# Optimization experiments

Measured on AMD Instinct MI355X. Metric: run time of the kernel, lower is better.

## Reference

```python
import jax, jax.numpy as jnp
import numpy as np

D = 128; T = 128; E = 100; H = 2
B = 2048; N0 = 3 * B; K0 = 5; N1 = N0 * K0; K1 = 10
NN = 200000; M = 4096; MSG = 2 * D + E + T  # 484


def t2v(t, w, b):
    # Time2Vec: cos(t * w + b), output [..., T]
    return jnp.cos(t[..., None] * w + b)


def gru_cell(x, h, Wih, bih, Whh, bhh):
    gi = x @ Wih.T + bih
    gh = h @ Whh.T + bhh
    ir, iz, inn = jnp.split(gi, 3, axis=-1)
    hr, hz, hn = jnp.split(gh, 3, axis=-1)
    r = jax.nn.sigmoid(ir + hr)
    u = jax.nn.sigmoid(iz + hz)
    n = jnp.tanh(inn + r * hn)
    return (1.0 - u) * n + u * h


def temporal_attn(node_feat, time_feat, edge_feat, nbr_feat, nbr_time_feat, mask,
                  Wq, bq, Wk, bk, Wv, bv, Wo, bo):
    N = node_feat.shape[0]
    q = (jnp.concatenate([node_feat, time_feat], -1) @ Wq + bq).reshape(N, H, D // H)
    kin = jnp.concatenate([nbr_feat, edge_feat, nbr_time_feat], -1)  # [N, K, D+E+T]
    k = (kin @ Wk + bk).reshape(N, -1, H, D // H)
    v = (kin @ Wv + bv).reshape(N, -1, H, D // H)
    s = jnp.einsum('nhd,nkhd->nhk', q, k) / jnp.sqrt(jnp.asarray(D // H, q.dtype))
    s = jnp.where(mask[:, None, :] > 0, s, jnp.asarray(-1e9, s.dtype))
    a = jax.nn.softmax(s, axis=-1)
    hout = jnp.einsum('nhk,nkhd->nhd', a, v).reshape(N, D)
    return jax.nn.relu(jnp.concatenate([hout, node_feat], -1) @ Wo + bo)


def setup_inputs() -> dict:
    key = jax.random.key(0)
    ks = jax.random.split(key, 60)
    it = iter(range(60))
    nx = lambda: ks[next(it)]
    p = lambda shape: jax.random.normal(nx(), shape, jnp.float32) * 0.05
    inp = dict(memory=p((NN, D)), time_w=p((T,)), time_b=p((T,)),
               gru_Wih=p((3 * D, MSG)), gru_bih=p((3 * D,)),
               gru_Whh=p((3 * D, D)), gru_bhh=p((3 * D,)))
    for l in (0, 1):
        inp['Wq%d' % l] = p((D + T, D)); inp['bq%d' % l] = p((D,))
        inp['Wk%d' % l] = p((D + E + T, D)); inp['bk%d' % l] = p((D,))
        inp['Wv%d' % l] = p((D + E + T, D)); inp['bv%d' % l] = p((D,))
        inp['Wo%d' % l] = p((2 * D, D)); inp['bo%d' % l] = p((D,))
    inp.update(lp_Ws=p((D, D)), lp_bs=p((D,)), lp_Wd=p((D, D)), lp_bd=p((D,)),
               lp_Wo=p((D, 1)), lp_bo=p((1,)))
    inp['msgs'] = jax.random.normal(nx(), (M, MSG), jnp.float32)
    inp['times0'] = jax.random.uniform(nx(), (N0,), jnp.float32) * 100.0 + 100.0
    inp['nbr_times0'] = inp['times0'][:, None] - jax.random.uniform(nx(), (N0, K0), jnp.float32) * 100.0
    inp['nbr_feats0'] = jax.random.normal(nx(), (N0, K0, E), jnp.float32)
    inp['times1'] = jax.random.uniform(nx(), (N1,), jnp.float32) * 100.0 + 100.0
    inp['nbr_times1'] = inp['times1'][:, None] - jax.random.uniform(nx(), (N1, K1), jnp.float32) * 100.0
    inp['nbr_feats1'] = jax.random.normal(nx(), (N1, K1, E), jnp.float32)
    inp['msg_nids'] = jax.random.permutation(nx(), NN)[:M].astype(jnp.int32)
    inp['seed0'] = jax.random.randint(nx(), (N0,), 0, NN, jnp.int32)
    inp['seed1'] = jax.random.randint(nx(), (N1,), 0, NN, jnp.int32)
    inp['nbr_local0'] = (N0 + jax.random.randint(nx(), (N0, K0), 0, N1)).astype(jnp.int32)
    inp['nbr_mask0'] = jax.random.randint(nx(), (N0, K0), 0, 2, jnp.int32).at[:, 0].set(1)
    inp['nbr_mask1'] = jax.random.randint(nx(), (N1, K1), 0, 2, jnp.int32).at[:, 0].set(1)
    inp['src_local'] = jax.random.randint(nx(), (B,), 0, N0, jnp.int32)
    inp['dst_local'] = jax.random.randint(nx(), (B,), 0, N0, jnp.int32)
    inp['neg_local'] = jax.random.randint(nx(), (B,), 0, N0, jnp.int32)
    return inp


def reference(memory, time_w, time_b, gru_Wih, gru_bih, gru_Whh, gru_bhh,
              Wq0, bq0, Wk0, bk0, Wv0, bv0, Wo0, bo0,
              Wq1, bq1, Wk1, bk1, Wv1, bv1, Wo1, bo1,
              lp_Ws, lp_bs, lp_Wd, lp_bd, lp_Wo, lp_bo,
              msgs, times0, nbr_times0, nbr_feats0, times1, nbr_times1, nbr_feats1,
              msg_nids, seed0, seed1, nbr_local0, nbr_mask0, nbr_mask1,
              src_local, dst_local, neg_local):
    # GRU memory update on aggregated messages (get_updated_memory)
    mem = memory.at[msg_nids].set(
        gru_cell(msgs, memory[msg_nids], gru_Wih, gru_bih, gru_Whh, gru_bhh))
    z = jnp.zeros((N0 + N1, D), jnp.float32)
    # hop 1 (outermost): neighbor node features are zeros
    tf1 = t2v(jnp.zeros((N1,), jnp.float32), time_w, time_b)
    ntf1 = t2v(times1[:, None] - nbr_times1, time_w, time_b)
    out1 = temporal_attn(mem[seed1], tf1, nbr_feats1,
                         jnp.zeros((N1, K1, D), jnp.float32), ntf1, nbr_mask1,
                         Wq1, bq1, Wk1, bk1, Wv1, bv1, Wo1, bo1)
    z = z.at[N0 + jnp.arange(N1)].set(out1)
    # hop 0: gather neighbor embeddings from hop-1 results
    tf0 = t2v(jnp.zeros((N0,), jnp.float32), time_w, time_b)
    ntf0 = t2v(times0[:, None] - nbr_times0, time_w, time_b)
    out0 = temporal_attn(mem[seed0], tf0, nbr_feats0, z[nbr_local0], ntf0, nbr_mask0,
                         Wq0, bq0, Wk0, bk0, Wv0, bv0, Wo0, bo0)
    z = z.at[jnp.arange(N0)].set(out0)
    z_src, z_dst, z_neg = z[src_local], z[dst_local], z[neg_local]

    def link_pred(a, c):
        hh = jax.nn.relu(a @ lp_Ws + lp_bs + c @ lp_Wd + lp_bd)
        return jax.nn.sigmoid(hh @ lp_Wo + lp_bo).ravel()

    return link_pred(z_src, z_dst), link_pred(z_src, z_neg)
```

## Files before the change

### kernel.cpp

```cpp
#include <hip/hip_runtime.h>
#include <math.h>

#define D    128
#define TT   128
#define E    100
#define NHD  2
#define BSZ  2048
#define N0C  6144
#define K0C  5
#define N1C  30720
#define K1C  10
#define NNC  200000
#define MC   4096
#define MSG  484
#define KIN  356
#define GK   612
#define GKP  616
#define GN   512

typedef __attribute__((ext_vector_type(8))) short short8v;
typedef __attribute__((ext_vector_type(4))) float f32x4;

__device__ __forceinline__ float sigmoidf_(float x){ return 1.f/(1.f+__expf(-x)); }
__device__ __forceinline__ unsigned short f2b(float f){
    unsigned int x = __float_as_uint(f);
    unsigned int r = (x + 0x7fffu + ((x>>16)&1u)) >> 16;
    return (unsigned short)r;
}
__device__ __forceinline__ float b2f(unsigned short u){
    return __uint_as_float(((unsigned int)u)<<16);
}

__global__ void k_pre_small(const float* time_b,
                            const float* Wq0,const float* bq0,const float* Wq1,const float* bq1,
                            const float* bv0,const float* Wo0,const float* bo0,
                            const float* bv1,const float* Wo1,const float* bo1,
                            float* qc0, float* qc1, float* cb0, float* cb1){
    __shared__ float cosb[TT];
    int j = threadIdx.x;
    cosb[j] = cosf(time_b[j]);
    __syncthreads();
    float a0=bq0[j], a1=bq1[j];
    for(int t=0;t<TT;++t){ a0 += cosb[t]*Wq0[(D+t)*D + j]; a1 += cosb[t]*Wq1[(D+t)*D + j]; }
    qc0[j]=a0; qc1[j]=a1;
    float c0=bo0[j], c1=bo1[j];
    for(int jp=0;jp<D;++jp){ c0 += bv0[jp]*Wo0[jp*D + j]; c1 += bv1[jp]*Wo1[jp*D + j]; }
    cb0[j]=c0; cb1[j]=c1;
}

__global__ void k_wf(const float* Wq,const float* Wk,const float* bk,const float* qc,
                     unsigned short* WF, float* cF, int cmin){
    int span = 356 - cmin;
    int hstr = span + 4;
    int width = 2*hstr;
    int idx = blockIdx.x;
    int h = idx / hstr; int cl = idx % hstr;
    int k = threadIdx.x;
    if(cl > span){
        WF[(size_t)k*width + idx] = (unsigned short)0;
        if(k==0) cF[idx] = 0.f;
        return;
    }
    int c = cmin + cl;
    float a = 0.f;
    for(int d=0; d<64; ++d){
        float wkv = (c < KIN) ? Wk[c*D + h*64+d] : bk[h*64+d];
        a += Wq[k*D + h*64+d] * wkv;
    }
    WF[(size_t)k*width + idx] = f2b(a);
    if(k==0){
        float s=0.f;
        for(int d=0; d<64; ++d){
            float wkv = (c < KIN) ? Wk[c*D + h*64+d] : bk[h*64+d];
            s += qc[h*64+d]*wkv;
        }
        cF[idx] = s;
    }
}

__global__ void k_bcat(const float* Wv, const float* Wo, unsigned short* Bcat, int cmin){
    int span = KIN - cmin; int rows = 2*span;
    int r = blockIdx.x; int j = threadIdx.x;
    float a;
    if(r < rows){
        int h = r/span; int c = cmin + (r - h*span);
        a = 0.f;
        for(int d=0; d<64; ++d) a += Wv[c*D + h*64+d] * Wo[(h*64+d)*D + j];
    } else {
        a = Wo[(size_t)(D + (r - rows))*D + j];
    }
    Bcat[(size_t)r*D + j] = f2b(a);
}

__global__ __launch_bounds__(256) void k_gruB(const float* Wih, const float* Whh, unsigned short* B){
    __shared__ float tile[64][65];
    int rb = blockIdx.x*64;
    int jb = blockIdx.y*64;
    int t = threadIdx.x;
    int rr = t&63, jj0 = t>>6;
    #pragma unroll
    for(int i=0;i<16;++i){
        int jj = jj0 + i*4;
        int j = jb + jj; int r = rb + rr;
        float v = 0.f;
        if(r < GK){
            if(j < 256)      v = (r<MSG)? Wih[(size_t)j*MSG+r] : Whh[(size_t)j*D + (r-MSG)];
            else if(j < 384) v = (r<MSG)? Wih[(size_t)j*MSG+r] : 0.f;
            else             v = (r<MSG)? 0.f : Whh[(size_t)(j-128)*D + (r-MSG)];
        }
        tile[jj][rr] = v;
    }
    __syncthreads();
    int jw = t&63, rr0 = t>>6;
    #pragma unroll
    for(int i=0;i<16;++i){
        int rr2 = rr0 + i*4;
        int r = rb + rr2;
        if(r < GK) B[(size_t)r*GN + jb + jw] = f2b(tile[jw][rr2]);
    }
}
__global__ void k_gruBias(const float* bih, const float* bhh, float* bias){
    int j = threadIdx.x + blockIdx.x*256;
    if(j >= GN) return;
    float v;
    if(j < 256)      v = bih[j] + bhh[j];
    else if(j < 384) v = bih[j];
    else             v = bhh[j-128];
    bias[j] = v;
}
__global__ void k_acvt(const float* msgs, const float* memory, const int* msg_nids,
                       unsigned short* ab, float* hprevf){
    int i = blockIdx.x*256 + threadIdx.x;
    if(i >= MC*GKP) return;
    int row = i / GKP; int c = i - row*GKP;
    float v;
    if(c < MSG) v = msgs[(size_t)row*MSG + c];
    else if(c < GK){ int d = c-MSG; v = memory[(size_t)msg_nids[row]*D + d]; hprevf[row*D+d] = v; }
    else v = 0.f;
    ab[i] = f2b(v);
}
__global__ void k_gates3(const float* part, const float* bias, const float* hprevf, float* upd){
    int i = blockIdx.x*256 + threadIdx.x;
    if(i >= MC*D) return;
    int row = i>>7, d = i&127;
    const float* p = part + (size_t)row*GN;
    const size_t S = (size_t)MC*GN;
    float gr = p[d]     + p[S+d]     + p[2*S+d]     + bias[d];
    float gu = p[128+d] + p[S+128+d] + p[2*S+128+d] + bias[128+d];
    float gi = p[256+d] + p[S+256+d] + p[2*S+256+d] + bias[256+d];
    float gh = p[384+d] + p[S+384+d] + p[2*S+384+d] + bias[384+d];
    float r = sigmoidf_(gr);
    float u = sigmoidf_(gu);
    float n = tanhf(gi + r*gh);
    upd[i] = (1.f-u)*n + u*hprevf[i];
}

__global__ void k_map_init(int* map){ int i = blockIdx.x*256+threadIdx.x; if(i<NNC) map[i] = -1; }
__global__ void k_map_scatter(const int* msg_nids, int* map){
    int i = blockIdx.x*256+threadIdx.x; if(i<MC) map[msg_nids[i]] = i;
}

__global__ void k_gatherf(const int* seed1,const int* seed0,const int* map,
                          const float* memory,const float* upd,
                          unsigned short* hb1, unsigned short* acat1,
                          unsigned short* hb0, unsigned short* acat0){
    int i = blockIdx.x*256 + threadIdx.x;
    const int total1 = N1C*D;
    int li; const int* seed; unsigned short* hb; unsigned short* acat; int ldav, hoff;
    if(i < total1){ li=i; seed=seed1; hb=hb1; acat=acat1; ldav=584; hoff=456; }
    else { li = i - total1; if(li >= N0C*D) return; seed=seed0; hb=hb0; acat=acat0; ldav=840; hoff=712; }
    int row = li>>7, c = li&127;
    int sid = seed[row];
    int mi = map[sid];
    float v = (mi>=0) ? upd[(size_t)mi*D + c] : memory[(size_t)sid*D + c];
    unsigned short u = f2b(v);
    hb[li] = u;
    acat[(size_t)row*ldav + hoff + c] = u;
}

template<int BM, int SPLITK, bool RELU, bool OUTF32>
__global__ __launch_bounds__(256) void k_gmm(const unsigned short* A, int lda,
                                             const unsigned short* B, int ldb,
                                             const float* bias, void* Cp, int ldc,
                                             int K, int N, int M){
    constexpr int ASTR = 72;
    constexpr int BSTR = 72;
    constexpr int RPW = BM/4;
    constexpr int RT  = RPW/16;
    constexpr int AIT = BM/32;
    __shared__ unsigned short As[BM*ASTR];
    __shared__ unsigned short Bs[64*BSTR];
    int t = threadIdx.x;
    int wave = t>>6, lane = t&63;
    int l15 = lane&15, l4 = lane>>4;
    int m0 = blockIdx.y*BM, n0 = blockIdx.x*64;
    int ntiles = (K+63)>>6;
    int tbeg, tend;
    if(SPLITK==1){ tbeg=0; tend=ntiles; }
    else {
        int tper = (ntiles + SPLITK-1)/SPLITK;
        tbeg = blockIdx.z*tper;
        tend = min(ntiles, tbeg+tper);
    }
    f32x4 acc[RT][4];
    #pragma unroll
    for(int rt=0;rt<RT;++rt)
        #pragma unroll
        for(int ct=0;ct<4;++ct) acc[rt][ct] = (f32x4){0.f,0.f,0.f,0.f};

    uint4 apre[AIT]; unsigned short bpre[16];
    auto loadA = [&](int kt){
        int k0 = kt<<6;
        #pragma unroll
        for(int i=0;i<AIT;++i){
            int idx = t + i*256;
            int row = idx>>3; int kc = (idx&7)*8;
            uint4 v = {0u,0u,0u,0u};
            if(k0+kc < K) v = *(const uint4*)(A + (size_t)(m0+row)*lda + k0 + kc);
            apre[i] = v;
        }
    };
    auto loadB = [&](int kt){
        int k0 = kt<<6;
        int n = t&63; int kb = (t>>6)*16;
        int ng = n0+n;
        #pragma unroll
        for(int j=0;j<16;++j){
            int kg = k0 + kb + j;
            bpre[j] = (kg<K && ng<N) ? B[(size_t)kg*ldb + ng] : (unsigned short)0;
        }
    };
    auto stash = [&](){
        #pragma unroll
        for(int i=0;i<AIT;++i){
            int idx = t + i*256;
            int row = idx>>3; int kc = (idx&7)*8;
            *(uint4*)&As[row*ASTR + kc] = apre[i];
        }
        int n = t&63; int kb = (t>>6)*16;
        #pragma unroll
        for(int j=0;j<16;++j) Bs[n*BSTR + kb + j] = bpre[j];
    };

    loadA(tbeg); loadB(tbeg);
    for(int kt=tbeg; kt<tend; ++kt){
        stash();
        __syncthreads();
        if(kt+1 < tend){ loadA(kt+1); loadB(kt+1); }
        #pragma unroll
        for(int kk=0; kk<64; kk+=32){
            short8v bfr[4];
            #pragma unroll
            for(int ct=0;ct<4;++ct)
                bfr[ct] = *(const short8v*)&Bs[(ct*16+l15)*BSTR + kk + l4*8];
            #pragma unroll
            for(int rt=0;rt<RT;++rt){
                short8v afr = *(const short8v*)&As[(wave*RPW + rt*16 + l15)*ASTR + kk + l4*8];
                #pragma unroll
                for(int ct=0;ct<4;++ct)
                    acc[rt][ct] = __builtin_amdgcn_mfma_f32_16x16x32_bf16(afr, bfr[ct], acc[rt][ct], 0,0,0);
            }
        }
        __syncthreads();
    }
    #pragma unroll
    for(int rt=0;rt<RT;++rt){
        #pragma unroll
        for(int ct=0;ct<4;++ct){
            int col = n0 + ct*16 + l15;
            if(col < N){
                #pragma unroll
                for(int r=0;r<4;++r){
                    int row = m0 + wave*RPW + rt*16 + l4*4 + r;
                    if(SPLITK==1){
                        float v = acc[rt][ct][r] + bias[col];
                        if(RELU) v = fmaxf(v, 0.f);
                        if(OUTF32) ((float*)Cp)[(size_t)row*ldc + col] = v;
                        else ((unsigned short*)Cp)[(size_t)row*ldc + col] = f2b(v);
                    } else {
                        ((float*)Cp)[((size_t)blockIdx.z*M + row)*ldc + col] = acc[rt][ct][r];
                    }
                }
            }
        }
    }
}

template<int SPL, bool RELU, bool OUTF32>
__global__ void k_kred(const float* part, int M, int N, const float* bias, void* out){
    int i = blockIdx.x*256 + threadIdx.x;
    if(i >= M*N) return;
    int col = i & (N-1);
    float v = bias[col];
    #pragma unroll
    for(int z=0;z<SPL;++z) v += part[(size_t)z*M*N + i];
    if(RELU) v = fmaxf(v, 0.f);
    if(OUTF32) ((float*)out)[i] = v;
    else ((unsigned short*)out)[i] = f2b(v);
}

template<int K, int CMIN, int S4, int NPW>
__global__ __launch_bounds__(256) void k_attn(const unsigned short* __restrict__ qwb,
    unsigned short* __restrict__ avout, int ldav,
    const float* __restrict__ times, const float* __restrict__ nbr_times,
    const float* __restrict__ nbr_feats,
    const int* __restrict__ nbr_mask, const int* __restrict__ nbr_local,
    const unsigned short* __restrict__ zbuf,
    const float* __restrict__ time_w, const float* __restrict__ time_b){
    constexpr int SPAN = KIN - CMIN;
    constexpr int QSTR = SPAN + 4;
    constexpr int QLD  = 2*QSTR;
    int wv = __builtin_amdgcn_readfirstlane(blockIdx.x*4 + (threadIdx.x>>6));
    int lane = threadIdx.x & 63;

    float4 tw4[S4], tb4[S4];
    #pragma unroll
    for(int s=0;s<S4;++s){
        int c = CMIN + s*256 + lane*4;
        if(c >= D+E && c < KIN){
            tw4[s] = *(const float4*)(time_w + (c-(D+E)));
            tb4[s] = *(const float4*)(time_b + (c-(D+E)));
        } else {
            tw4[s] = make_float4(0.f,0.f,0.f,0.f);
            tb4[s] = make_float4(0.f,0.f,0.f,0.f);
        }
    }

    #pragma unroll
    for(int i=0;i<NPW;++i){
        int n = wv*NPW + i;
        const unsigned short* qrow = qwb + (size_t)n*QLD;
        float tn = times[n];
        int   mk[K]; float tk[K]; int nl[K];
        #pragma unroll
        for(int k=0;k<K;++k){
            mk[k] = nbr_mask [(size_t)n*K + k];
            tk[k] = nbr_times[(size_t)n*K + k];
            nl[k] = (CMIN==0) ? nbr_local[(size_t)n*K + k] : 0;
        }

        float4 qw4[NHD][S4]; float qb[NHD];
        #pragma unroll
        for(int h=0;h<NHD;++h){
            qb[h] = b2f(qrow[h*QSTR + SPAN]);
            #pragma unroll
            for(int s=0;s<S4;++s){
                int cl = s*256 + lane*4;
                float4 v = make_float4(0.f,0.f,0.f,0.f);
                if(cl < SPAN){
                    uint2 w = *(const uint2*)(qrow + h*QSTR + cl);
                    v.x = __uint_as_float(w.x<<16);
                    v.y = __uint_as_float(w.x & 0xffff0000u);
                    v.z = __uint_as_float(w.y<<16);
                    v.w = __uint_as_float(w.y & 0xffff0000u);
                }
                qw4[h][s] = v;
            }
        }

        float4 kin4[K][S4];
        #pragma unroll
        for(int k=0;k<K;++k){
            float dt = tn - tk[k];
            const float* ef = nbr_feats + (size_t)(n*K+k)*E;
            const unsigned short* zf = (CMIN==0) ?
                (zbuf + (size_t)(nl[k] - N0C)*D) : (const unsigned short*)0;
            #pragma unroll
            for(int s=0;s<S4;++s){
                int c = CMIN + s*256 + lane*4;
                float4 kv = make_float4(0.f,0.f,0.f,0.f);
                if(c < KIN){
                    if(CMIN==0 && c < D){
                        uint2 w = *(const uint2*)(zf + c);
                        kv.x = __uint_as_float(w.x<<16);
                        kv.y = __uint_as_float(w.x & 0xffff0000u);
                        kv.z = __uint_as_float(w.y<<16);
                        kv.w = __uint_as_float(w.y & 0xffff0000u);
                    } else if(c < D+E){
                        kv = *(const float4*)(ef + (c-D));
                    } else {
                        kv.x = __cosf(dt*tw4[s].x + tb4[s].x);
                        kv.y = __cosf(dt*tw4[s].y + tb4[s].y);
                        kv.z = __cosf(dt*tw4[s].z + tb4[s].z);
                        kv.w = __cosf(dt*tw4[s].w + tb4[s].w);
                    }
                }
                kin4[k][s] = kv;
            }
        }

        float p0[K], p1[K];
        #pragma unroll
        for(int k=0;k<K;++k){
            float a0 = 0.f, a1 = 0.f;
            #pragma unroll
            for(int s=0;s<S4;++s){
                float4 kv = kin4[k][s];
                a0 += kv.x*qw4[0][s].x + kv.y*qw4[0][s].y + kv.z*qw4[0][s].z + kv.w*qw4[0][s].w;
                a1 += kv.x*qw4[1][s].x + kv.y*qw4[1][s].y + kv.z*qw4[1][s].z + kv.w*qw4[1][s].w;
            }
            p0[k] = a0; p1[k] = a1;
        }

        #pragma unroll
        for(int off=32; off; off>>=1){
            #pragma unroll
            for(int k=0;k<K;++k){
                p0[k] += __shfl_xor(p0[k], off);
                p1[k] += __shfl_xor(p1[k], off);
            }
        }

        float sval[NHD][K];
        #pragma unroll
        for(int k=0;k<K;++k){
            bool act = mk[k] > 0;
            sval[0][k] = act ? (p0[k] + qb[0])*0.125f : -1e9f;
            sval[1][k] = act ? (p1[k] + qb[1])*0.125f : -1e9f;
        }
        #pragma unroll
        for(int h=0;h<NHD;++h){
            float mx = -1e30f;
            #pragma unroll
            for(int k=0;k<K;++k) mx = fmaxf(mx, sval[h][k]);
            float z=0.f;
            #pragma unroll
            for(int k=0;k<K;++k){ float e = __expf(sval[h][k]-mx); sval[h][k]=e; z+=e; }
            float inv = 1.f/z;
            #pragma unroll
            for(int k=0;k<K;++k) sval[h][k]*=inv;
        }
        #pragma unroll
        for(int h=0;h<NHD;++h)
          #pragma unroll
          for(int s=0;s<S4;++s){
            int cl = s*256 + lane*4;
            if(cl < SPAN){
                float v0=0.f,v1=0.f,v2=0.f,v3=0.f;
                #pragma unroll
                for(int k=0;k<K;++k){
                    float a = sval[h][k];
                    v0 += a*kin4[k][s].x; v1 += a*kin4[k][s].y;
                    v2 += a*kin4[k][s].z; v3 += a*kin4[k][s].w;
                }
                uint2 o;
                o.x = (unsigned int)f2b(v0) | ((unsigned int)f2b(v1)<<16);
                o.y = (unsigned int)f2b(v2) | ((unsigned int)f2b(v3)<<16);
                *(uint2*)(avout + (size_t)n*ldav + h*SPAN + cl) = o;
            }
          }
    }
}

__global__ __launch_bounds__(128) void k_linkpred(const float* z0,
      const int* src,const int* dst,const int* neg,
      const float* Ws,const float* bs,const float* Wd,const float* bd,
      const float* Wo,const float* bo, float* out){
    __shared__ float zs[D], zd[D], zn[D];
    __shared__ float red[4];
    int b = blockIdx.x; int d = threadIdx.x;
    zs[d] = z0[(size_t)src[b]*D + d];
    zd[d] = z0[(size_t)dst[b]*D + d];
    zn[d] = z0[(size_t)neg[b]*D + d];
    __syncthreads();
    float ss=0.f, sdd=0.f, snn=0.f;
    for(int c=0;c<D;++c){
        float w1 = Ws[c*D + d], w2 = Wd[c*D + d];
        ss  += zs[c]*w1; sdd += zd[c]*w2; snn += zn[c]*w2;
    }
    float bb = bs[d] + bd[d];
    float h1 = fmaxf(ss + sdd + bb, 0.f);
    float h2 = fmaxf(ss + snn + bb, 0.f);
    float w = Wo[d];
    float v1 = h1*w, v2 = h2*w;
    #pragma unroll
    for(int off=32; off; off>>=1){ v1 += __shfl_xor(v1,off); v2 += __shfl_xor(v2,off); }
    int wid = d>>6;
    if((d&63)==0){ red[wid*2]=v1; red[wid*2+1]=v2; }
    __syncthreads();
    if(d==0){
        out[b]       = sigmoidf_(red[0]+red[2] + bo[0]);
        out[BSZ + b] = sigmoidf_(red[1]+red[3] + bo[0]);
    }
}

extern "C" void kernel_launch(void* const* d_in, const int* in_sizes, int n_in,
                              void* d_out, int out_size, void* d_ws, size_t ws_size,
                              hipStream_t stream) {
    const float* memory  = (const float*)d_in[0];
    const float* time_w  = (const float*)d_in[1];
    const float* time_b  = (const float*)d_in[2];
    const float* gWih    = (const float*)d_in[3];
    const float* gbih    = (const float*)d_in[4];
    const float* gWhh    = (const float*)d_in[5];
    const float* gbhh    = (const float*)d_in[6];
    const float* Wq0=(const float*)d_in[7],  *bq0=(const float*)d_in[8];
    const float* Wk0=(const float*)d_in[9],  *bk0=(const float*)d_in[10];
    const float* Wv0=(const float*)d_in[11], *bv0=(const float*)d_in[12];
    const float* Wo0=(const float*)d_in[13], *bo0=(const float*)d_in[14];
    const float* Wq1=(const float*)d_in[15], *bq1=(const float*)d_in[16];
    const float* Wk1=(const float*)d_in[17], *bk1=(const float*)d_in[18];
    const float* Wv1=(const float*)d_in[19], *bv1=(const float*)d_in[20];
    const float* Wo1=(const float*)d_in[21], *bo1=(const float*)d_in[22];
    const float* lpWs=(const float*)d_in[23], *lpbs=(const float*)d_in[24];
    const float* lpWd=(const float*)d_in[25], *lpbd=(const float*)d_in[26];
    const float* lpWo=(const float*)d_in[27], *lpbo=(const float*)d_in[28];
    const float* msgs    = (const float*)d_in[29];
    const float* times0  = (const float*)d_in[30];
    const float* ntimes0 = (const float*)d_in[31];
    const float* nfeats0 = (const float*)d_in[32];
    const float* times1  = (const float*)d_in[33];
    const float* ntimes1 = (const float*)d_in[34];
    const float* nfeats1 = (const float*)d_in[35];
    const int* msg_nids  = (const int*)d_in[36];
    const int* seed0     = (const int*)d_in[37];
    const int* seed1     = (const int*)d_in[38];
    const int* nbr_local0= (const int*)d_in[39];
    const int* nbr_mask0 = (const int*)d_in[40];
    const int* nbr_mask1 = (const int*)d_in[41];
    const int* src       = (const int*)d_in[42];
    const int* dst       = (const int*)d_in[43];
    const int* neg       = (const int*)d_in[44];

    char* ws = (char*)d_ws;
    size_t off = 0;
    auto alloc = [&](size_t bytes)->char*{
        char* p = ws + off;
        off += (bytes + 255) & ~(size_t)255;
        return p;
    };
    int*   map   = (int*)  alloc((size_t)NNC*4);
    float* upd   = (float*)alloc((size_t)MC*D*4);
    unsigned short* hb1   = (unsigned short*)alloc((size_t)N1C*D*2);
    unsigned short* qwb1  = (unsigned short*)alloc((size_t)N1C*464*2);
    unsigned short* acat1 = (unsigned short*)alloc((size_t)N1C*584*2);
    unsigned short* zb1   = (unsigned short*)alloc((size_t)N1C*D*2);
    unsigned short* hb0   = (unsigned short*)alloc((size_t)N0C*D*2);
    unsigned short* qwb0  = (unsigned short*)alloc((size_t)N0C*720*2);
    unsigned short* acat0 = (unsigned short*)alloc((size_t)N0C*840*2);
    float* z0    = (float*)alloc((size_t)N0C*D*4);
    float* qc0   = (float*)alloc(512);
    float* qc1   = (float*)alloc(512);
    float* cb0   = (float*)alloc(512);
    float* cb1   = (float*)alloc(512);
    unsigned short* WFb0 = (unsigned short*)alloc((size_t)D*720*2);
    unsigned short* WFb1 = (unsigned short*)alloc((size_t)D*464*2);
    float* cF0   = (float*)alloc((size_t)720*4);
    float* cF1   = (float*)alloc((size_t)464*4);
    unsigned short* Bcat1 = (unsigned short*)alloc((size_t)584*D*2);
    unsigned short* Bcat0 = (unsigned short*)alloc((size_t)840*D*2);
    unsigned short* gA    = (unsigned short*)alloc((size_t)MC*GKP*2);
    unsigned short* gB    = (unsigned short*)alloc((size_t)GK*GN*2);
    float* gBias = (float*)alloc((size_t)GN*4);
    float* hprevf= (float*)alloc((size_t)MC*D*4);
    float* part  = (float*)alloc((size_t)2*N1C*D*4);
    float* outp = (float*)d_out;

    k_pre_small<<<1,128,0,stream>>>(time_b, Wq0,bq0,Wq1,bq1, bv0,Wo0,bo0, bv1,Wo1,bo1,
                                    qc0,qc1,cb0,cb1);
    k_wf<<<720,128,0,stream>>>(Wq0,Wk0,bk0,qc0, WFb0,cF0, 0);
    k_wf<<<464,128,0,stream>>>(Wq1,Wk1,bk1,qc1, WFb1,cF1, 128);
    k_bcat<<<584,128,0,stream>>>(Wv1, Wo1, Bcat1, 128);
    k_bcat<<<840,128,0,stream>>>(Wv0, Wo0, Bcat0, 0);
    k_gruB<<<dim3(10,8),256,0,stream>>>(gWih, gWhh, gB);
    k_gruBias<<<2,256,0,stream>>>(gbih, gbhh, gBias);

    k_map_init<<<(NNC+255)/256,256,0,stream>>>(map);
    k_map_scatter<<<MC/256,256,0,stream>>>(msg_nids, map);
    k_acvt<<<(MC*GKP+255)/256,256,0,stream>>>(msgs, memory, msg_nids, gA, hprevf);
    k_gmm<128,3,false,true><<<dim3(GN/64, MC/128, 3),256,0,stream>>>(gA,GKP, gB,GN, gBias, part,GN, GK, GN, MC);
    k_gates3<<<(MC*D+255)/256,256,0,stream>>>(part, gBias, hprevf, upd);

    k_gatherf<<<((N1C+N0C)*D)/256,256,0,stream>>>(seed1, seed0, map, memory, upd,
                                                  hb1, acat1, hb0, acat0);

    k_gmm<128,1,false,false><<<dim3(8,  N1C/128),256,0,stream>>>(hb1,128, WFb1,464, cF1, qwb1,464, 128, 464, N1C);
    k_gmm<128,1,false,false><<<dim3(12, N0C/128),256,0,stream>>>(hb0,128, WFb0,720, cF0, qwb0,720, 128, 720, N0C);

    k_attn<K1C,128,1,1><<<N1C/4,256,0,stream>>>(qwb1, acat1, 584, times1, ntimes1, nfeats1,
                                                nbr_mask1, (const int*)0, (const unsigned short*)0,
                                                time_w, time_b);
    k_gmm<128,2,true,false><<<dim3(2, N1C/128, 2),256,0,stream>>>(acat1,584, Bcat1,D, cb1, part,D, 584, D, N1C);
    k_kred<2,true,false><<<(N1C*D+255)/256,256,0,stream>>>(part, N1C, D, cb1, zb1);

    k_attn<K0C,0,2,1><<<N0C/4,256,0,stream>>>(qwb0, acat0, 840, times0, ntimes0, nfeats0,
                                              nbr_mask0, nbr_local0, zb1,
                                              time_w, time_b);
    k_gmm<64,4,true,true><<<dim3(2, N0C/64, 4),256,0,stream>>>(acat0,840, Bcat0,D, cb0, part,D, 840, D, N0C);
    k_kred<4,true,true><<<(N0C*D+255)/256,256,0,stream>>>(part, N0C, D, cb0, z0);

    k_linkpred<<<BSZ,128,0,stream>>>(z0, src,dst,neg, lpWs,lpbs,lpWd,lpbd, lpWo,lpbo, outp);
}
```

Before: 559.0 us.

## Stage attention keys in LDS, skip masked neighbors, drop map-init kernels

The attention kernel now stores the per-neighbor key/input vectors in shared memory instead of a large register array. It declares launch bounds to allow four blocks per SM and skips score and value accumulation for masked neighbors, using a valid neighbor index for loads. The node-to-message map no longer needs a full 200k-entry initialization: it is scattered inside the bf16 conversion kernel and validated in the gather by checking msg_nids[map[sid]] == sid. The GRU bias kernel is folded into the small precompute kernel to cut launches. Together these aim to cut register pressure and launch overhead, at the cost of extra LDS traffic and a validation read per gather.

```diff
diff --git a/kernel.cpp b/kernel.cpp
--- a/kernel.cpp
+++ b/kernel.cpp
@@ -35,17 +35,27 @@
                             const float* Wq0,const float* bq0,const float* Wq1,const float* bq1,
                             const float* bv0,const float* Wo0,const float* bo0,
                             const float* bv1,const float* Wo1,const float* bo1,
+                            const float* bih,const float* bhh,float* gBias,
                             float* qc0, float* qc1, float* cb0, float* cb1){
     __shared__ float cosb[TT];
     int j = threadIdx.x;
-    cosb[j] = cosf(time_b[j]);
+    if(j < TT) cosb[j] = cosf(time_b[j]);
     __syncthreads();
-    float a0=bq0[j], a1=bq1[j];
-    for(int t=0;t<TT;++t){ a0 += cosb[t]*Wq0[(D+t)*D + j]; a1 += cosb[t]*Wq1[(D+t)*D + j]; }
-    qc0[j]=a0; qc1[j]=a1;
-    float c0=bo0[j], c1=bo1[j];
-    for(int jp=0;jp<D;++jp){ c0 += bv0[jp]*Wo0[jp*D + j]; c1 += bv1[jp]*Wo1[jp*D + j]; }
-    cb0[j]=c0; cb1[j]=c1;
+    if(j < 128){
+        float a0=bq0[j], a1=bq1[j];
+        for(int t=0;t<TT;++t){ a0 += cosb[t]*Wq0[(D+t)*D + j]; a1 += cosb[t]*Wq1[(D+t)*D + j]; }
+        qc0[j]=a0; qc1[j]=a1;
+        float c0=bo0[j], c1=bo1[j];
+        for(int jp=0;jp<D;++jp){ c0 += bv0[jp]*Wo0[jp*D + j]; c1 += bv1[jp]*Wo1[jp*D + j]; }
+        cb0[j]=c0; cb1[j]=c1;
+    }
+    if(j < GN){
+        float v;
+        if(j < 256)      v = bih[j] + bhh[j];
+        else if(j < 384) v = bih[j];
+        else             v = bhh[j-128];
+        gBias[j] = v;
+    }
 }
 
 __global__ void k_wf(const float* Wq,const float* Wk,const float* bk,const float* qc,
@@ -119,20 +129,12 @@
         if(r < GK) B[(size_t)r*GN + jb + jw] = f2b(tile[jw][rr2]);
     }
 }
-__global__ void k_gruBias(const float* bih, const float* bhh, float* bias){
-    int j = threadIdx.x + blockIdx.x*256;
-    if(j >= GN) return;
-    float v;
-    if(j < 256)      v = bih[j] + bhh[j];
-    else if(j < 384) v = bih[j];
-    else             v = bhh[j-128];
-    bias[j] = v;
-}
 __global__ void k_acvt(const float* msgs, const float* memory, const int* msg_nids,
-                       unsigned short* ab, float* hprevf){
+                       unsigned short* ab, float* hprevf, int* map){
     int i = blockIdx.x*256 + threadIdx.x;
     if(i >= MC*GKP) return;
     int row = i / GKP; int c = i - row*GKP;
+    if(c == 0) map[msg_nids[row]] = row;
     float v;
     if(c < MSG) v = msgs[(size_t)row*MSG + c];
     else if(c < GK){ int d = c-MSG; v = memory[(size_t)msg_nids[row]*D + d]; hprevf[row*D+d] = v; }
@@ -155,12 +157,7 @@
     upd[i] = (1.f-u)*n + u*hprevf[i];
 }
 
-__global__ void k_map_init(int* map){ int i = blockIdx.x*256+threadIdx.x; if(i<NNC) map[i] = -1; }
-__global__ void k_map_scatter(const int* msg_nids, int* map){
-    int i = blockIdx.x*256+threadIdx.x; if(i<MC) map[msg_nids[i]] = i;
-}
-
-__global__ void k_gatherf(const int* seed1,const int* seed0,const int* map,
+__global__ void k_gatherf(const int* seed1,const int* seed0,const int* map,const int* msg_nids,
                           const float* memory,const float* upd,
                           unsigned short* hb1, unsigned short* acat1,
                           unsigned short* hb0, unsigned short* acat0){
@@ -172,7 +169,8 @@
     int row = li>>7, c = li&127;
     int sid = seed[row];
     int mi = map[sid];
-    float v = (mi>=0) ? upd[(size_t)mi*D + c] : memory[(size_t)sid*D + c];
+    bool valid = ((unsigned)mi < (unsigned)MC) && (msg_nids[mi] == sid);
+    float v = valid ? upd[(size_t)mi*D + c] : memory[(size_t)sid*D + c];
     unsigned short u = f2b(v);
     hb[li] = u;
     acat[(size_t)row*ldav + hoff + c] = u;
@@ -300,7 +298,7 @@
 }
 
 template<int K, int CMIN, int S4, int NPW>
-__global__ __launch_bounds__(256) void k_attn(const unsigned short* __restrict__ qwb,
+__global__ __launch_bounds__(256,4) void k_attn(const unsigned short* __restrict__ qwb,
     unsigned short* __restrict__ avout, int ldav,
     const float* __restrict__ times, const float* __restrict__ nbr_times,
     const float* __restrict__ nbr_feats,
@@ -310,8 +308,11 @@
     constexpr int SPAN = KIN - CMIN;
     constexpr int QSTR = SPAN + 4;
     constexpr int QLD  = 2*QSTR;
-    int wv = __builtin_amdgcn_readfirstlane(blockIdx.x*4 + (threadIdx.x>>6));
+    __shared__ float4 kls[4*K*S4*64];
+    int w = threadIdx.x>>6;
+    int wv = __builtin_amdgcn_readfirstlane(blockIdx.x*4 + w);
     int lane = threadIdx.x & 63;
+    float4* myk = kls + w*(K*S4*64);
 
     float4 tw4[S4], tb4[S4];
     #pragma unroll
@@ -348,34 +349,34 @@
                 int cl = s*256 + lane*4;
                 float4 v = make_float4(0.f,0.f,0.f,0.f);
                 if(cl < SPAN){
-                    uint2 w = *(const uint2*)(qrow + h*QSTR + cl);
-                    v.x = __uint_as_float(w.x<<16);
-                    v.y = __uint_as_float(w.x & 0xffff0000u);
-                    v.z = __uint_as_float(w.y<<16);
-                    v.w = __uint_as_float(w.y & 0xffff0000u);
+                    uint2 wq = *(const uint2*)(qrow + h*QSTR + cl);
+                    v.x = __uint_as_float(wq.x<<16);
+                    v.y = __uint_as_float(wq.x & 0xffff0000u);
+                    v.z = __uint_as_float(wq.y<<16);
+                    v.w = __uint_as_float(wq.y & 0xffff0000u);
                 }
                 qw4[h][s] = v;
             }
         }
 
-        float4 kin4[K][S4];
         #pragma unroll
         for(int k=0;k<K;++k){
-            float dt = tn - tk[k];
-            const float* ef = nbr_feats + (size_t)(n*K+k)*E;
+            int gk = (mk[k] > 0) ? k : 0;
+            float dt = tn - tk[gk];
+            const float* ef = nbr_feats + (size_t)(n*K+gk)*E;
             const unsigned short* zf = (CMIN==0) ?
-                (zbuf + (size_t)(nl[k] - N0C)*D) : (const unsigned short*)0;
+                (zbuf + (size_t)(nl[gk] - N0C)*D) : (const unsigned short*)0;
             #pragma unroll
             for(int s=0;s<S4;++s){
                 int c = CMIN + s*256 + lane*4;
                 float4 kv = make_float4(0.f,0.f,0.f,0.f);
                 if(c < KIN){
                     if(CMIN==0 && c < D){
-                        uint2 w = *(const uint2*)(zf + c);
-                        kv.x = __uint_as_float(w.x<<16);
-                        kv.y = __uint_as_float(w.x & 0xffff0000u);
-                        kv.z = __uint_as_float(w.y<<16);
-                        kv.w = __uint_as_float(w.y & 0xffff0000u);
+                        uint2 wz = *(const uint2*)(zf + c);
+                        kv.x = __uint_as_float(wz.x<<16);
+                        kv.y = __uint_as_float(wz.x & 0xffff0000u);
+                        kv.z = __uint_as_float(wz.y<<16);
+                        kv.w = __uint_as_float(wz.y & 0xffff0000u);
                     } else if(c < D+E){
                         kv = *(const float4*)(ef + (c-D));
                     } else {
@@ -385,21 +386,25 @@
                         kv.w = __cosf(dt*tw4[s].w + tb4[s].w);
                     }
                 }
-                kin4[k][s] = kv;
+                myk[(k*S4+s)*64 + lane] = kv;
             }
         }
 
         float p0[K], p1[K];
         #pragma unroll
+        for(int k=0;k<K;++k){ p0[k]=0.f; p1[k]=0.f; }
+        #pragma unroll
         for(int k=0;k<K;++k){
-            float a0 = 0.f, a1 = 0.f;
-            #pragma unroll
-            for(int s=0;s<S4;++s){
-                float4 kv = kin4[k][s];
-                a0 += kv.x*qw4[0][s].x + kv.y*qw4[0][s].y + kv.z*qw4[0][s].z + kv.w*qw4[0][s].w;
-                a1 += kv.x*qw4[1][s].x + kv.y*qw4[1][s].y + kv.z*qw4[1][s].z + kv.w*qw4[1][s].w;
+            if(mk[k] > 0){
+                float a0 = 0.f, a1 = 0.f;
+                #pragma unroll
+                for(int s=0;s<S4;++s){
+                    float4 kv = myk[(k*S4+s)*64 + lane];
+                    a0 += kv.x*qw4[0][s].x + kv.y*qw4[0][s].y + kv.z*qw4[0][s].z + kv.w*qw4[0][s].w;
+                    a1 += kv.x*qw4[1][s].x + kv.y*qw4[1][s].y + kv.z*qw4[1][s].z + kv.w*qw4[1][s].w;
+                }
+                p0[k] = a0; p1[k] = a1;
             }
-            p0[k] = a0; p1[k] = a1;
         }
 
         #pragma unroll
@@ -430,25 +435,31 @@
             #pragma unroll
             for(int k=0;k<K;++k) sval[h][k]*=inv;
         }
-        #pragma unroll
-        for(int h=0;h<NHD;++h)
-          #pragma unroll
-          for(int s=0;s<S4;++s){
+
+        #pragma unroll
+        for(int s=0;s<S4;++s){
             int cl = s*256 + lane*4;
             if(cl < SPAN){
-                float v0=0.f,v1=0.f,v2=0.f,v3=0.f;
+                float a00=0.f,a01=0.f,a02=0.f,a03=0.f;
+                float a10=0.f,a11=0.f,a12=0.f,a13=0.f;
                 #pragma unroll
                 for(int k=0;k<K;++k){
-                    float a = sval[h][k];
-                    v0 += a*kin4[k][s].x; v1 += a*kin4[k][s].y;
-                    v2 += a*kin4[k][s].z; v3 += a*kin4[k][s].w;
+                    if(mk[k] > 0){
+                        float4 kv = myk[(k*S4+s)*64 + lane];
+                        float w0 = sval[0][k], w1 = sval[1][k];
+                        a00 += w0*kv.x; a01 += w0*kv.y; a02 += w0*kv.z; a03 += w0*kv.w;
+                        a10 += w1*kv.x; a11 += w1*kv.y; a12 += w1*kv.z; a13 += w1*kv.w;
+                    }
                 }
-                uint2 o;
-                o.x = (unsigned int)f2b(v0) | ((unsigned int)f2b(v1)<<16);
-                o.y = (unsigned int)f2b(v2) | ((unsigned int)f2b(v3)<<16);
-                *(uint2*)(avout + (size_t)n*ldav + h*SPAN + cl) = o;
+                uint2 o0, o1;
+                o0.x = (unsigned int)f2b(a00) | ((unsigned int)f2b(a01)<<16);
+                o0.y = (unsigned int)f2b(a02) | ((unsigned int)f2b(a03)<<16);
+                o1.x = (unsigned int)f2b(a10) | ((unsigned int)f2b(a11)<<16);
+                o1.y = (unsigned int)f2b(a12) | ((unsigned int)f2b(a13)<<16);
+                *(uint2*)(avout + (size_t)n*ldav + cl)        = o0;
+                *(uint2*)(avout + (size_t)n*ldav + SPAN + cl) = o1;
             }
-          }
+        }
     }
 }
 
@@ -556,22 +567,19 @@
     float* part  = (float*)alloc((size_t)2*N1C*D*4);
     float* outp = (float*)d_out;
 
-    k_pre_small<<<1,128,0,stream>>>(time_b, Wq0,bq0,Wq1,bq1, bv0,Wo0,bo0, bv1,Wo1,bo1,
-                                    qc0,qc1,cb0,cb1);
+    k_pre_small<<<1,512,0,stream>>>(time_b, Wq0,bq0,Wq1,bq1, bv0,Wo0,bo0, bv1,Wo1,bo1,
+                                    gbih, gbhh, gBias, qc0,qc1,cb0,cb1);
     k_wf<<<720,128,0,stream>>>(Wq0,Wk0,bk0,qc0, WFb0,cF0, 0);
     k_wf<<<464,128,0,stream>>>(Wq1,Wk1,bk1,qc1, WFb1,cF1, 128);
     k_bcat<<<584,128,0,stream>>>(Wv1, Wo1, Bcat1, 128);
     k_bcat<<<840,128,0,stream>>>(Wv0, Wo0, Bcat0, 0);
     k_gruB<<<dim3(10,8),256,0,stream>>>(gWih, gWhh, gB);
-    k_gruBias<<<2,256,0,stream>>>(gbih, gbhh, gBias);
-
-    k_map_init<<<(NNC+255)/256,256,0,stream>>>(map);
-    k_map_scatter<<<MC/256,256,0,stream>>>(msg_nids, map);
-    k_acvt<<<(MC*GKP+255)/256,256,0,stream>>>(msgs, memory, msg_nids, gA, hprevf);
+
+    k_acvt<<<(MC*GKP+255)/256,256,0,stream>>>(msgs, memory, msg_nids, gA, hprevf, map);
     k_gmm<128,3,false,true><<<dim3(GN/64, MC/128, 3),256,0,stream>>>(gA,GKP, gB,GN, gBias, part,GN, GK, GN, MC);
     k_gates3<<<(MC*D+255)/256,256,0,stream>>>(part, gBias, hprevf, upd);
 
-    k_gatherf<<<((N1C+N0C)*D)/256,256,0,stream>>>(seed1, seed0, map, memory, upd,
+    k_gatherf<<<((N1C+N0C)*D)/256,256,0,stream>>>(seed1, seed0, map, msg_nids, memory, upd,
                                                   hb1, acat1, hb0, acat0);
 
     k_gmm<128,1,false,false><<<dim3(8,  N1C/128),256,0,stream>>>(hb1,128, WFb1,464, cF1, qwb1,464, 128, 464, N1C);
```

Result: slower. 590.9 us (+5.7%).
